# Kernel tuning notes

Hardware: AMD Instinct MI355X
Metric: run time of the kernel (lower is better)

The kernel has to match this reference:

```python
import jax, jax.numpy as jnp
import numpy as np

D = 1024   # n_embd
H = 16     # n_head
NL = 6     # n_layer
B = 16
L = 64
T = 3 * L  # interleaved (rtg, state, action) tokens
NB = 100   # rtg bucket number
DF = 4 * D


def _ln(x, g, b, eps=1e-5):
    mu = jnp.mean(x, -1, keepdims=True)
    var = jnp.mean((x - mu) ** 2, -1, keepdims=True)
    return (x - mu) * jax.lax.rsqrt(var + eps) * g + b


def _gelu(x):
    return jax.nn.gelu(x, approximate=False)  # matches torch F.gelu (erf)


def setup_inputs() -> dict:
    key = jax.random.key(0)
    ks = iter(jax.random.split(key, 64))
    def rn(shape, s=0.02):
        return jax.random.normal(next(ks), shape, jnp.float32) * s
    inp = dict(
        states=jax.random.normal(next(ks), (B, L, 91), jnp.float32),
        actions=jax.random.normal(next(ks), (B, L, 1, 27), jnp.float32),
        rtgs=jax.random.uniform(next(ks), (B, L), jnp.float32) * 100.0,
        attention_mask=jnp.ones((B, L), bool),
        y_len=L,
        # state encoder: Linear(91,D) GELU Linear(D,D) GELU
        se_w1=rn((91, D)), se_b1=jnp.zeros(D), se_w2=rn((D, D)), se_b2=jnp.zeros(D),
        # action encoder: Linear(27,D) GELU Linear(D,D)
        ae_w1=rn((27, D)), ae_b1=jnp.zeros(D), ae_w2=rn((D, D)), ae_b2=jnp.zeros(D),
        # Autodis
        ad_bucket_w=rn((1, D)), ad_bucket_b=jnp.zeros(D), ad_ret_w=rn((1, NB)), ad_res_w=rn((NB, NB)),
        pos_emb=rn((1, T, D)),
        # transformer blocks (stacked over layers)
        ln1_g=jnp.ones((NL, D)), ln1_b=jnp.zeros((NL, D)),
        Wq=rn((NL, D, D)), bq=jnp.zeros((NL, D)),
        Wk=rn((NL, D, D)), bk=jnp.zeros((NL, D)),
        Wv=rn((NL, D, D)), bv=jnp.zeros((NL, D)),
        Wp=rn((NL, D, D)), bp=jnp.zeros((NL, D)),
        ln2_g=jnp.ones((NL, D)), ln2_b=jnp.zeros((NL, D)),
        Wm1=rn((NL, D, DF)), bm1=jnp.zeros((NL, DF)),
        Wm2=rn((NL, DF, D)), bm2=jnp.zeros((NL, D)),
        lin_w=rn((D, 27)), lin_b=jnp.zeros(27),
    )
    return inp


def _forward(attention_mask, states, actions, rtgs, se_w1, se_b1, se_w2, se_b2,
             ae_w1, ae_b1, ae_w2, ae_b2, ad_bucket_w, ad_bucket_b, ad_ret_w, ad_res_w,
             pos_emb, ln1_g, ln1_b, Wq, bq, Wk, bk, Wv, bv, Wp, bp,
             ln2_g, ln2_b, Wm1, bm1, Wm2, bm2, lin_w, lin_b):
    Bsz, Ls = states.shape[0], states.shape[1]
    Ts = 3 * Ls
    hd = D // H
    # encoders
    state_emb = _gelu(_gelu(states @ se_w1 + se_b1) @ se_w2 + se_b2)          # [B,L,D]
    act = actions[:, :, 0, :]                                                  # squeeze(2) -> [B,L,27]
    action_emb = _gelu(act @ ae_w1 + ae_b1) @ ae_w2 + ae_b2                    # [B,L,D]
    # Autodis rtg embedding
    bucket_value = jnp.linspace(0.0, 100.0, NB).reshape(NB, 1)
    meta = bucket_value @ ad_bucket_w + ad_bucket_b                            # [NB,D]
    s = jax.nn.leaky_relu(rtgs[..., None] @ ad_ret_w)                          # [B,L,NB]
    s = s + s @ ad_res_w
    e = jnp.exp(s - jnp.max(s, -1, keepdims=True))
    p = e / (1e-8 + jnp.sum(e, -1, keepdims=True))
    rtg_emb = p @ meta                                                         # [B,L,D]
    # interleave rtg/state/action tokens -> [B,3L,D]
    tok = jnp.stack([rtg_emb, state_emb, action_emb], axis=2).reshape(Bsz, Ts, D)
    x = tok + pos_emb[:, :Ts]
    # combined padding + causal mask
    m = jnp.repeat(attention_mask, 3, axis=1)                                  # [B,3L]
    causal = jnp.tril(jnp.ones((Ts, Ts), bool))
    fmask = m[:, None, :, None] & m[:, None, None, :] & causal[None, None]     # [B,1,T,T]
    scale = 1.0 / np.sqrt(hd)
    for i in range(NL):
        h = _ln(x, ln1_g[i], ln1_b[i])
        q = (h @ Wq[i] + bq[i]).reshape(Bsz, Ts, H, hd).transpose(0, 2, 1, 3)
        k = (h @ Wk[i] + bk[i]).reshape(Bsz, Ts, H, hd).transpose(0, 2, 1, 3)
        v = (h @ Wv[i] + bv[i]).reshape(Bsz, Ts, H, hd).transpose(0, 2, 1, 3)
        att = jnp.einsum('bhid,bhjd->bhij', q, k) * scale
        att = jnp.where(fmask, att, -1e9)
        att = jax.nn.softmax(att, axis=-1)
        y = jnp.einsum('bhij,bhjd->bhid', att, v).transpose(0, 2, 1, 3).reshape(Bsz, Ts, D)
        x = x + (y @ Wp[i] + bp[i])
        h2 = _ln(x, ln2_g[i], ln2_b[i])
        x = x + _gelu(h2 @ Wm1[i] + bm1[i]) @ Wm2[i] + bm2[i]
    return x @ lin_w + lin_b                                                   # [B,3L,27]


def reference(states, actions, rtgs, attention_mask, y_len, se_w1, se_b1, se_w2, se_b2,
              ae_w1, ae_b1, ae_w2, ae_b2, ad_bucket_w, ad_bucket_b, ad_ret_w, ad_res_w,
              pos_emb, ln1_g, ln1_b, Wq, bq, Wk, bk, Wv, bv, Wp, bp,
              ln2_g, ln2_b, Wm1, bm1, Wm2, bm2, lin_w, lin_b):
    return _forward(attention_mask, states, actions, rtgs, se_w1, se_b1, se_w2, se_b2,
                    ae_w1, ae_b1, ae_w2, ae_b2, ad_bucket_w, ad_bucket_b, ad_ret_w, ad_res_w,
                    pos_emb, ln1_g, ln1_b, Wq, bq, Wk, bk, Wv, bv, Wp, bp,
                    ln2_g, ln2_b, Wm1, bm1, Wm2, bm2, lin_w, lin_b)
```

## Files before the change

### kernel.cpp

```cpp
#include <hip/hip_runtime.h>
#include <cmath>

typedef unsigned short u16;
typedef unsigned int   u32;
typedef short s16x8 __attribute__((ext_vector_type(8)));
typedef float f32x4 __attribute__((ext_vector_type(4)));

#define D_  1024
#define H_  16
#define NL_ 6
#define B_  16
#define L_  64
#define T_  192
#define NB_ 100
#define DF_ 4096
#define BT_ (B_*T_)
#define BL_ (B_*L_)

__device__ __forceinline__ float b2f(u16 u){ u32 x = ((u32)u)<<16; return __uint_as_float(x); }
__device__ __forceinline__ u16 f2b(float f){ u32 x = __float_as_uint(f); x += 0x7fffu + ((x>>16)&1u); return (u16)(x>>16); }
__device__ __forceinline__ float gelu_f(float v){ return 0.5f*v*(1.0f+erff(v*0.70710678118f)); }

typedef const unsigned int __attribute__((address_space(1)))* as1_u32p;
typedef unsigned int __attribute__((address_space(3)))* as3_u32p;
__device__ __forceinline__ void gload16(const void* g, void* l)
{
    __builtin_amdgcn_global_load_lds((as1_u32p)g, (as3_u32p)l, 16, 0, 0);
}

__device__ __forceinline__ void tconv_tile(const float* __restrict__ W,
                                           u16* __restrict__ Wt,
                                           int K, int N, int nb, int kb, int tid)
{
    __shared__ float tile[64][65];
    int tr = tid >> 4, tc = tid & 15;
#pragma unroll
    for (int rr = 0; rr < 4; ++rr) {
        int k = tr + rr*16;
        float4 v = *(const float4*)(W + (size_t)(kb + k)*N + nb + tc*4);
        tile[k][tc*4+0] = v.x; tile[k][tc*4+1] = v.y;
        tile[k][tc*4+2] = v.z; tile[k][tc*4+3] = v.w;
    }
    __syncthreads();
#pragma unroll
    for (int rr = 0; rr < 4; ++rr) {
        int n = tr + rr*16;
        ushort4 o;
        o.x = f2b(tile[tc*4+0][n]);
        o.y = f2b(tile[tc*4+1][n]);
        o.z = f2b(tile[tc*4+2][n]);
        o.w = f2b(tile[tc*4+3][n]);
        *(ushort4*)(Wt + (size_t)(nb + n)*K + kb + tc*4) = o;
    }
}

__global__ __launch_bounds__(256) void tconv_kernel(const float* __restrict__ W,
                                                    u16* __restrict__ Wt,
                                                    int K, int N)
{
    tconv_tile(W, Wt, K, N, blockIdx.x*64, blockIdx.y*64, threadIdx.x);
}

__global__ __launch_bounds__(256) void tconvL_kernel(const float* __restrict__ Wq,
                                                     const float* __restrict__ Wk,
                                                     const float* __restrict__ Wv,
                                                     const float* __restrict__ Wp,
                                                     const float* __restrict__ Wm1,
                                                     const float* __restrict__ Wm2,
                                                     u16* __restrict__ Wqkvt,
                                                     u16* __restrict__ Wpt,
                                                     u16* __restrict__ Wm1t,
                                                     u16* __restrict__ Wm2t,
                                                     int layer)
{
    size_t DD = (size_t)D_*D_, DDF = (size_t)D_*DF_;
    int t = blockIdx.x;
    if (t < 1024) {
        int sel = t >> 8, tt = t & 255;
        const float* Wz = ((sel == 0) ? Wq : (sel == 1) ? Wk : (sel == 2) ? Wv : Wp) + layer*DD;
        u16* Wtz = (sel == 3) ? (Wpt + layer*DD) : (Wqkvt + layer*3*DD + sel*DD);
        tconv_tile(Wz, Wtz, D_, D_, (tt & 15)*64, (tt >> 4)*64, threadIdx.x);
    } else if (t < 2048) {
        int t2 = t - 1024;
        tconv_tile(Wm1 + layer*DDF, Wm1t + layer*DDF, D_, DF_, (t2 & 63)*64, (t2 >> 6)*64, threadIdx.x);
    } else {
        int t2 = t - 2048;
        tconv_tile(Wm2 + layer*DDF, Wm2t + layer*DDF, DF_, D_, (t2 & 15)*64, (t2 >> 4)*64, threadIdx.x);
    }
}

__global__ __launch_bounds__(256) void pack_qkv_bias_kernel(const float* __restrict__ bq,
                                                            const float* __restrict__ bk,
                                                            const float* __restrict__ bv,
                                                            float* __restrict__ out)
{
    int i = blockIdx.x*256 + threadIdx.x;
    int layer = i / 3072;
    int r = i - layer*3072;
    int c = r >> 10, d = r & 1023;
    const float* src = (c == 0) ? bq : (c == 1) ? bk : bv;
    out[i] = src[layer*1024 + d];
}

__global__ __launch_bounds__(256) void tlin_kernel(const float* __restrict__ w,
                                                   float* __restrict__ wt)
{
    int k = blockIdx.x*256 + threadIdx.x;
#pragma unroll 1
    for (int c = 0; c < 27; ++c)
        wt[c*1024 + k] = w[k*27 + c];
}

__global__ __launch_bounds__(256) void embed1_kernel(const float* __restrict__ A,
                                                     const float* __restrict__ W,
                                                     const float* __restrict__ bias,
                                                     u16* __restrict__ out, int K)
{
    int idx = blockIdx.x*256 + threadIdx.x;
    int m = idx >> 10, n = idx & 1023;
    float acc = bias[n];
    for (int k = 0; k < K; ++k)
        acc += A[m*K + k] * W[k*1024 + n];
    out[idx] = f2b(gelu_f(acc));
}

__global__ __launch_bounds__(128) void rtg_kernel(const float* __restrict__ rtgs,
                                                  const float* __restrict__ ret_w,
                                                  const float* __restrict__ res_w,
                                                  const float* __restrict__ bucket_w,
                                                  const float* __restrict__ bucket_b,
                                                  float* __restrict__ eR)
{
    int r = blockIdx.x, tid = threadIdx.x;
    __shared__ float sarr[NB_];
    __shared__ float red[128];
    float rtg = rtgs[r];
    float s = 0.f;
    if (tid < NB_) {
        float v = rtg * ret_w[tid];
        s = (v > 0.f) ? v : 0.01f*v;
        sarr[tid] = s;
    }
    __syncthreads();
    float s2 = -1e30f;
    if (tid < NB_) {
        float acc = s;
        for (int m = 0; m < NB_; ++m) acc += sarr[m] * res_w[m*NB_ + tid];
        s2 = acc;
    }
    red[tid] = s2; __syncthreads();
    for (int off = 64; off > 0; off >>= 1) { if (tid < off) red[tid] = fmaxf(red[tid], red[tid+off]); __syncthreads(); }
    float mx = red[0]; __syncthreads();
    float e = (tid < NB_) ? expf(s2 - mx) : 0.f;
    red[tid] = e; __syncthreads();
    for (int off = 64; off > 0; off >>= 1) { if (tid < off) red[tid] += red[tid+off]; __syncthreads(); }
    float S = red[0]; __syncthreads();
    float bv = (100.f/99.f) * (float)tid;
    red[tid] = e * bv; __syncthreads();
    for (int off = 64; off > 0; off >>= 1) { if (tid < off) red[tid] += red[tid+off]; __syncthreads(); }
    float EB = red[0];
    float inv = 1.f/(1e-8f + S);
    float c = EB * inv, sg = S * inv;
    for (int d = tid; d < D_; d += 128)
        eR[(size_t)r*D_ + d] = c*bucket_w[d] + sg*bucket_b[d];
}

__global__ __launch_bounds__(256) void assemble_kernel(const float* __restrict__ eR,
                                                       const float* __restrict__ eS,
                                                       const float* __restrict__ eA,
                                                       const float* __restrict__ pos,
                                                       float* __restrict__ xf)
{
    int idx = blockIdx.x*256 + threadIdx.x;
    int row = idx >> 10, d = idx & 1023;
    int b = row / T_, t = row % T_;
    int l = t / 3, c = t % 3;
    const float* src = (c == 0) ? eR : (c == 1) ? eS : eA;
    xf[idx] = src[(size_t)(b*L_ + l)*D_ + d] + pos[(size_t)t*D_ + d];
}

template<int NP>
__global__ __launch_bounds__(256) void ln_kernel(const float* __restrict__ x,
                                                 const float* __restrict__ parts,
                                                 size_t pstride,
                                                 const float* __restrict__ g,
                                                 const float* __restrict__ bb,
                                                 float* __restrict__ xout,
                                                 u16* __restrict__ out)
{
    int row = blockIdx.x*4 + (threadIdx.x >> 6);
    int lane = threadIdx.x & 63;
    const float4* xr = (const float4*)(x + (size_t)row*D_);
    float4 v[4];
    float s = 0.f, q = 0.f;
#pragma unroll
    for (int i = 0; i < 4; ++i) {
        float4 a = xr[lane + i*64];
        if (NP == 4) {
#pragma unroll
            for (int z = 0; z < 4; ++z) {
                float4 p = ((const float4*)(parts + (size_t)z*pstride + (size_t)row*D_))[lane + i*64];
                a.x += p.x; a.y += p.y; a.z += p.z; a.w += p.w;
            }
        }
        v[i] = a;
        s += a.x+a.y+a.z+a.w;
        q += a.x*a.x+a.y*a.y+a.z*a.z+a.w*a.w;
    }
    if (NP == 4) {
#pragma unroll
        for (int i = 0; i < 4; ++i)
            ((float4*)(xout + (size_t)row*D_))[lane + i*64] = v[i];
    }
#pragma unroll
    for (int off = 1; off < 64; off <<= 1) {
        s += __shfl_xor(s, off, 64);
        q += __shfl_xor(q, off, 64);
    }
    float mean = s*(1.f/(float)D_);
    float var  = q*(1.f/(float)D_) - mean*mean;
    float rstd = rsqrtf(var + 1e-5f);
#pragma unroll
    for (int i = 0; i < 4; ++i) {
        int d0 = (lane + i*64)*4;
        ushort4 ov;
        ov.x = f2b((v[i].x-mean)*rstd*g[d0+0] + bb[d0+0]);
        ov.y = f2b((v[i].y-mean)*rstd*g[d0+1] + bb[d0+1]);
        ov.z = f2b((v[i].z-mean)*rstd*g[d0+2] + bb[d0+2]);
        ov.w = f2b((v[i].w-mean)*rstd*g[d0+3] + bb[d0+3]);
        ((ushort4*)(out + (size_t)row*D_))[lane + i*64] = ov;
    }
}

template<int GELU_ACT, int SPLITK, int ATOMIC>
__global__ __launch_bounds__(256) void gemm_bt(const u16* __restrict__ A,
                                               const u16* __restrict__ Bt,
                                               const float* __restrict__ bias,
                                               float* __restrict__ outF,
                                               u16* __restrict__ outB,
                                               int M, int N, int K, int kc,
                                               size_t partStride)
{
    __shared__ __align__(16) u16 As[3*128*32];
    __shared__ __align__(16) u16 Bs[3*128*32];
    int tid = threadIdx.x;

    int gx = gridDim.x;
    int nwg = gx * gridDim.y;
    int id = blockIdx.y * gx + blockIdx.x;
    int q8 = nwg >> 3;
    int nid = (id & 7) * q8 + (id >> 3);
    int n0 = (nid % gx) * 128;
    int m0 = (nid / gx) * 128;

    int wave = tid >> 6, lane = tid & 63;
    int wm = (wave >> 1) * 64, wn = (wave & 1) * 64;
    int lr = lane & 15, lq = lane >> 4;
    int slotRd = (lq ^ ((lr >> 1) & 3)) * 8;

    int srow = tid >> 2;
    int sslot = (tid & 3) ^ ((srow >> 1) & 3);

    int k0 = (SPLITK > 1) ? blockIdx.z * kc : 0;
    int nIt = ((SPLITK > 1) ? kc : K) >> 5;

    const u16* ap0 = A  + (size_t)(m0 + srow) * K + k0 + sslot * 8;
    const u16* ap1 = ap0 + (size_t)64 * K;
    const u16* bp0 = Bt + (size_t)(n0 + srow) * K + k0 + sslot * 8;
    const u16* bp1 = bp0 + (size_t)64 * K;

    u16 *sA0 = As, *sA1 = As + 4096, *sA2 = As + 8192;
    u16 *sB0 = Bs, *sB1 = Bs + 4096, *sB2 = Bs + 8192;
    int woff = wave * 512;

    f32x4 acc[4][4];
#pragma unroll
    for (int i = 0; i < 4; ++i)
#pragma unroll
        for (int j = 0; j < 4; ++j) acc[i][j] = (f32x4){0.f,0.f,0.f,0.f};

    gload16(ap0, sA0 + woff); gload16(ap1, sA0 + 2048 + woff);
    gload16(bp0, sB0 + woff); gload16(bp1, sB0 + 2048 + woff);
    ap0 += 32; ap1 += 32; bp0 += 32; bp1 += 32;
    gload16(ap0, sA1 + woff); gload16(ap1, sA1 + 2048 + woff);
    gload16(bp0, sB1 + woff); gload16(bp1, sB1 + 2048 + woff);
    ap0 += 32; ap1 += 32; bp0 += 32; bp1 += 32;

    for (int it = 0; it < nIt; ++it) {
        if (it + 1 < nIt) asm volatile("s_waitcnt vmcnt(4)" ::: "memory");
        else              asm volatile("s_waitcnt vmcnt(0)" ::: "memory");
        asm volatile("s_barrier" ::: "memory");
        if (it + 2 < nIt) {
            gload16(ap0, sA2 + woff); gload16(ap1, sA2 + 2048 + woff);
            gload16(bp0, sB2 + woff); gload16(bp1, sB2 + 2048 + woff);
            ap0 += 32; ap1 += 32; bp0 += 32; bp1 += 32;
        }
        s16x8 af[4], bf[4];
#pragma unroll
        for (int i = 0; i < 4; ++i)
            af[i] = *(const s16x8*)(sA0 + (wm + i*16 + lr)*32 + slotRd);
#pragma unroll
        for (int j = 0; j < 4; ++j)
            bf[j] = *(const s16x8*)(sB0 + (wn + j*16 + lr)*32 + slotRd);
#pragma unroll
        for (int i = 0; i < 4; ++i)
#pragma unroll
            for (int j = 0; j < 4; ++j)
                acc[i][j] = __builtin_amdgcn_mfma_f32_16x16x32_bf16(af[i], bf[j], acc[i][j], 0, 0, 0);
        u16* t0 = sA0; sA0 = sA1; sA1 = sA2; sA2 = t0;
        u16* t1 = sB0; sB0 = sB1; sB1 = sB2; sB2 = t1;
    }

    float* outZ = (SPLITK > 1 && !ATOMIC) ? outF + (size_t)blockIdx.z * partStride : outF;
#pragma unroll
    for (int i = 0; i < 4; ++i) {
        int mbase = m0 + wm + i*16 + lq*4;
#pragma unroll
        for (int j = 0; j < 4; ++j) {
            int n = n0 + wn + j*16 + lr;
            float bvl = (SPLITK > 1) ? ((blockIdx.z == 0) ? bias[n] : 0.f) : bias[n];
#pragma unroll
            for (int r = 0; r < 4; ++r) {
                int m = mbase + r;
                float v = acc[i][j][r] + bvl;
                size_t off = (size_t)m*N + n;
                if (SPLITK > 1) {
                    if (ATOMIC) atomicAdd(outF + off, v);
                    else        outZ[off] = v;
                } else {
                    if (GELU_ACT) v = gelu_f(v);
                    if (outF) outF[off] = v;
                    if (outB) outB[off] = f2b(v);
                }
            }
        }
    }
}

__global__ __launch_bounds__(256) void attn_mfma_kernel(const u16* __restrict__ qkv,
                                                        u16* __restrict__ yb)
{
    __shared__ __align__(16) u16 Vt[64*200];
    __shared__ __align__(16) u16 Pch[4][16*40];

    int tid = threadIdx.x;
    int b = blockIdx.x >> 4, h = blockIdx.x & 15;
    int c = blockIdx.y;
    int nrows = (c + 1) * 64;
    int bT = b * T_;
    int colBase = h * 64;
    int w = tid >> 6, lane = tid & 63;
    int lr = lane & 15, lq = lane >> 4;
    const int S3 = 3 * D_;

    for (int it = 0; it < (nrows >> 5); ++it) {
        int cc = it*256 + tid;
        int row = cc >> 3, ch = cc & 7;
        union { int4 v; u16 s[8]; } rv;
        rv.v = *(const int4*)(qkv + (size_t)(bT+row)*S3 + 2*D_ + colBase + ch*8);
#pragma unroll
        for (int i2 = 0; i2 < 8; ++i2)
            Vt[(ch*8 + i2)*200 + row] = rv.s[i2];
    }

    u16* Ch = Pch[w];
    int qt = c*4 + w;
    int tqb = qt * 16;

    const u16* qrow = qkv + (size_t)(bT + tqb + lr)*S3 + colBase + lq*8;
    s16x8 af0 = *(const s16x8*)(qrow);
    s16x8 af1 = *(const s16x8*)(qrow + 32);

    f32x4 sacc[12];
#pragma unroll
    for (int jt = 0; jt < 12; ++jt) {
        if (jt <= qt) {
            const u16* kr = qkv + (size_t)(bT + jt*16 + lr)*S3 + D_ + colBase + lq*8;
            s16x8 bk0 = *(const s16x8*)(kr);
            s16x8 bk1 = *(const s16x8*)(kr + 32);
            f32x4 a = (f32x4){0.f,0.f,0.f,0.f};
            a = __builtin_amdgcn_mfma_f32_16x16x32_bf16(af0, bk0, a, 0, 0, 0);
            a = __builtin_amdgcn_mfma_f32_16x16x32_bf16(af1, bk1, a, 0, 0, 0);
            sacc[jt] = a;
        }
    }

    float mrow[4] = {-1e30f,-1e30f,-1e30f,-1e30f};
#pragma unroll
    for (int jt = 0; jt < 12; ++jt) if (jt <= qt) {
#pragma unroll
        for (int r = 0; r < 4; ++r) {
            bool valid = (jt < qt) || (lr <= lq*4 + r);
            float s = valid ? sacc[jt][r]*0.125f : -1e30f;
            sacc[jt][r] = s;
            mrow[r] = fmaxf(mrow[r], s);
        }
    }
#pragma unroll
    for (int r = 0; r < 4; ++r) {
#pragma unroll
        for (int off = 1; off < 16; off <<= 1)
            mrow[r] = fmaxf(mrow[r], __shfl_xor(mrow[r], off, 64));
    }

    float lrow[4] = {0.f,0.f,0.f,0.f};
#pragma unroll
    for (int jt = 0; jt < 12; ++jt) if (jt <= qt) {
#pragma unroll
        for (int r = 0; r < 4; ++r) {
            float e = __expf(sacc[jt][r] - mrow[r]);
            sacc[jt][r] = e;
            lrow[r] += e;
        }
    }
#pragma unroll
    for (int r = 0; r < 4; ++r) {
#pragma unroll
        for (int off = 1; off < 16; off <<= 1)
            lrow[r] += __shfl_xor(lrow[r], off, 64);
        lrow[r] = 1.f / lrow[r];
    }

    __syncthreads();

    int nkt = (qt + 2) >> 1;
    f32x4 oacc[4];
#pragma unroll
    for (int nt = 0; nt < 4; ++nt) oacc[nt] = (f32x4){0.f,0.f,0.f,0.f};

#pragma unroll
    for (int kt = 0; kt < 6; ++kt) if (kt < nkt) {
        int jt0 = 2*kt, jt1 = 2*kt + 1;
#pragma unroll
        for (int r = 0; r < 4; ++r) {
            u16 e0 = f2b(sacc[jt0][r]);
            u16 e1 = (jt1 <= qt) ? f2b(sacc[jt1][r]) : (u16)0;
            Ch[(lq*4 + r)*40 + lr]      = e0;
            Ch[(lq*4 + r)*40 + 16 + lr] = e1;
        }
        s16x8 ap = *(const s16x8*)(Ch + lr*40 + lq*8);
#pragma unroll
        for (int nt = 0; nt < 4; ++nt) {
            s16x8 bv = *(const s16x8*)(Vt + (nt*16 + lr)*200 + kt*32 + lq*8);
            oacc[nt] = __builtin_amdgcn_mfma_f32_16x16x32_bf16(ap, bv, oacc[nt], 0, 0, 0);
        }
    }

#pragma unroll
    for (int nt = 0; nt < 4; ++nt)
#pragma unroll
        for (int r = 0; r < 4; ++r)
            yb[(size_t)(bT + tqb + lq*4 + r)*D_ + colBase + nt*16 + lr] =
                f2b(oacc[nt][r] * lrow[r]);
}

template<int NP>
__global__ __launch_bounds__(256) void final_kernel(const float* __restrict__ xf,
                                                    const float* __restrict__ parts,
                                                    size_t pstride,
                                                    const float* __restrict__ lin_wT,
                                                    const float* __restrict__ lin_b,
                                                    float* __restrict__ out)
{
    int row = blockIdx.x*4 + (threadIdx.x >> 6);
    int lane = threadIdx.x & 63;
    const float4* xr = (const float4*)(xf + (size_t)row*D_);
    float4 x[4];
#pragma unroll
    for (int i = 0; i < 4; ++i) {
        float4 v = xr[lane + i*64];
        if (NP == 4) {
#pragma unroll
            for (int z = 0; z < 4; ++z) {
                float4 p = ((const float4*)(parts + (size_t)z*pstride + (size_t)row*D_))[lane + i*64];
                v.x += p.x; v.y += p.y; v.z += p.z; v.w += p.w;
            }
        }
        x[i] = v;
    }
#pragma unroll 1
    for (int c = 0; c < 27; ++c) {
        const float4* wr = (const float4*)(lin_wT + (size_t)c*D_);
        float a = 0.f;
#pragma unroll
        for (int i = 0; i < 4; ++i) {
            float4 wv = wr[lane + i*64];
            a += x[i].x*wv.x + x[i].y*wv.y + x[i].z*wv.z + x[i].w*wv.w;
        }
#pragma unroll
        for (int off = 1; off < 64; off <<= 1)
            a += __shfl_xor(a, off, 64);
        if (lane == 0) out[(size_t)row*27 + c] = a + lin_b[c];
    }
}

extern "C" void kernel_launch(void* const* d_in, const int* in_sizes, int n_in,
                              void* d_out, int out_size, void* d_ws, size_t ws_size,
                              hipStream_t stream)
{
    const float* states   = (const float*)d_in[0];
    const float* actions  = (const float*)d_in[1];
    const float* rtgs     = (const float*)d_in[2];
    const float* se_w1 = (const float*)d_in[5];
    const float* se_b1 = (const float*)d_in[6];
    const float* se_w2 = (const float*)d_in[7];
    const float* se_b2 = (const float*)d_in[8];
    const float* ae_w1 = (const float*)d_in[9];
    const float* ae_b1 = (const float*)d_in[10];
    const float* ae_w2 = (const float*)d_in[11];
    const float* ae_b2 = (const float*)d_in[12];
    const float* ad_bucket_w = (const float*)d_in[13];
    const float* ad_bucket_b = (const float*)d_in[14];
    const float* ad_ret_w = (const float*)d_in[15];
    const float* ad_res_w = (const float*)d_in[16];
    const float* pos_emb  = (const float*)d_in[17];
    const float* ln1_g = (const float*)d_in[18];
    const float* ln1_b = (const float*)d_in[19];
    const float* Wq = (const float*)d_in[20];
    const float* bq = (const float*)d_in[21];
    const float* Wk = (const float*)d_in[22];
    const float* bk = (const float*)d_in[23];
    const float* Wv = (const float*)d_in[24];
    const float* bv = (const float*)d_in[25];
    const float* Wp = (const float*)d_in[26];
    const float* bp = (const float*)d_in[27];
    const float* ln2_g = (const float*)d_in[28];
    const float* ln2_b = (const float*)d_in[29];
    const float* Wm1 = (const float*)d_in[30];
    const float* bm1 = (const float*)d_in[31];
    const float* Wm2 = (const float*)d_in[32];
    const float* bm2 = (const float*)d_in[33];
    const float* lin_w = (const float*)d_in[34];
    const float* lin_b = (const float*)d_in[35];

    char* w = (char*)d_ws;
    auto take = [&](size_t bytes) { char* p = w; w += (bytes + 255) & ~(size_t)255; return p; };

    float* xf   = (float*)take((size_t)BT_*D_*4);
    u16* hb     = (u16*)take((size_t)BT_*D_*2);
    u16* qkvb   = (u16*)take((size_t)BT_*3*D_*2);
    char* scr   =        take((size_t)BT_*DF_*2);
    u16*  midb  = (u16*)scr;
    u16*  tSb   = (u16*)scr;
    u16*  tAb   = (u16*)(scr + (size_t)BL_*D_*2);
    float* eS   = (float*)(scr + (size_t)2*BL_*D_*2);
    float* eA   = (float*)(scr + (size_t)2*BL_*D_*2 + (size_t)BL_*D_*4);
    float* eR   = (float*)(scr + (size_t)2*BL_*D_*2 + (size_t)2*BL_*D_*4);
    float* pp   = (float*)take((size_t)4*BT_*D_*4);
    float* mq   = (float*)take((size_t)4*BT_*D_*4);

    u16* Wqkvt = (u16*)take((size_t)NL_*3*D_*D_*2);
    u16* Wpt   = (u16*)take((size_t)NL_*D_*D_*2);
    u16* Wm1t  = (u16*)take((size_t)NL_*D_*DF_*2);
    u16* Wm2t  = (u16*)take((size_t)NL_*DF_*D_*2);
    u16* sw2t  = (u16*)take((size_t)D_*D_*2);
    u16* aw2t  = (u16*)take((size_t)D_*D_*2);
    float* bqkv= (float*)take((size_t)NL_*3*D_*4);
    float* lwT = (float*)take((size_t)27*D_*4);

    size_t ask = (size_t)(w - (char*)d_ws);
    bool bigWS = (ws_size >= ask);

    const size_t PSTRIDE = (size_t)BT_*D_;
    size_t DD = (size_t)D_*D_, DDF = (size_t)D_*DF_;

    pack_qkv_bias_kernel<<<72, 256, 0, stream>>>(bq, bk, bv, bqkv);
    tlin_kernel<<<4, 256, 0, stream>>>(lin_w, lwT);
    tconv_kernel<<<dim3(16,16), 256, 0, stream>>>(se_w2, sw2t, D_, D_);
    tconv_kernel<<<dim3(16,16), 256, 0, stream>>>(ae_w2, aw2t, D_, D_);
    tconvL_kernel<<<3072, 256, 0, stream>>>(Wq, Wk, Wv, Wp, Wm1, Wm2,
                                            Wqkvt, Wpt, Wm1t, Wm2t, 0);

    embed1_kernel<<<4096, 256, 0, stream>>>(states,  se_w1, se_b1, tSb, 91);
    embed1_kernel<<<4096, 256, 0, stream>>>(actions, ae_w1, ae_b1, tAb, 27);
    gemm_bt<1,1,0><<<dim3(8,8), 256, 0, stream>>>(tSb, sw2t, se_b2, eS, nullptr, BL_, D_, D_, D_, 0);
    gemm_bt<0,1,0><<<dim3(8,8), 256, 0, stream>>>(tAb, aw2t, ae_b2, eA, nullptr, BL_, D_, D_, D_, 0);
    rtg_kernel<<<BL_, 128, 0, stream>>>(rtgs, ad_ret_w, ad_res_w, ad_bucket_w, ad_bucket_b, eR);
    assemble_kernel<<<(BT_*D_)/256, 256, 0, stream>>>(eR, eS, eA, pos_emb, xf);

    for (int i = 0; i < NL_; ++i) {
        if (i > 0 && bigWS)
            ln_kernel<4><<<BT_/4, 256, 0, stream>>>(xf, mq, PSTRIDE, ln1_g + i*D_, ln1_b + i*D_, xf, hb);
        else
            ln_kernel<0><<<BT_/4, 256, 0, stream>>>(xf, nullptr, 0, ln1_g + i*D_, ln1_b + i*D_, nullptr, hb);
        gemm_bt<0,1,0><<<dim3(24,24), 256, 0, stream>>>(hb, Wqkvt + (size_t)i*3*DD, bqkv + i*3*D_,
                                                        nullptr, qkvb, BT_, 3*D_, D_, D_, 0);
        attn_mfma_kernel<<<dim3(B_*H_,3), 256, 0, stream>>>(qkvb, hb);
        if (i + 1 < NL_)
            tconvL_kernel<<<3072, 256, 0, stream>>>(Wq, Wk, Wv, Wp, Wm1, Wm2,
                                                    Wqkvt, Wpt, Wm1t, Wm2t, i+1);
        if (bigWS)
            gemm_bt<0,4,0><<<dim3(8,24,4), 256, 0, stream>>>(hb, Wpt + (size_t)i*DD, bp + i*D_,
                                                             pp, nullptr, BT_, D_, D_, 256, PSTRIDE);
        else
            gemm_bt<0,2,1><<<dim3(8,24,2), 256, 0, stream>>>(hb, Wpt + (size_t)i*DD, bp + i*D_,
                                                             xf, nullptr, BT_, D_, D_, 512, 0);
        if (bigWS)
            ln_kernel<4><<<BT_/4, 256, 0, stream>>>(xf, pp, PSTRIDE, ln2_g + i*D_, ln2_b + i*D_, xf, hb);
        else
            ln_kernel<0><<<BT_/4, 256, 0, stream>>>(xf, nullptr, 0, ln2_g + i*D_, ln2_b + i*D_, nullptr, hb);
        gemm_bt<1,1,0><<<dim3(32,24), 256, 0, stream>>>(hb, Wm1t + (size_t)i*DDF, bm1 + i*DF_,
                                                        nullptr, midb, BT_, DF_, D_, D_, 0);
        if (bigWS)
            gemm_bt<0,4,0><<<dim3(8,24,4), 256, 0, stream>>>(midb, Wm2t + (size_t)i*DDF, bm2 + i*D_,
                                                             mq, nullptr, BT_, D_, DF_, 1024, PSTRIDE);
        else
            gemm_bt<0,2,1><<<dim3(8,24,2), 256, 0, stream>>>(midb, Wm2t + (size_t)i*DDF, bm2 + i*D_,
                                                             xf, nullptr, BT_, D_, DF_, 2048, 0);
    }

    if (bigWS)
        final_kernel<4><<<BT_/4, 256, 0, stream>>>(xf, mq, PSTRIDE, lwT, lin_b, (float*)d_out);
    else
        final_kernel<0><<<BT_/4, 256, 0, stream>>>(xf, nullptr, 0, lwT, lin_b, (float*)d_out);
}
```

Before: 1.557 ms.

## Store split-K partials in bf16 and stage attention K tile in LDS

```diff
diff --git a/kernel.cpp b/kernel.cpp
--- a/kernel.cpp
+++ b/kernel.cpp
@@ -181,7 +181,7 @@
 
 template<int NP>
 __global__ __launch_bounds__(256) void ln_kernel(const float* __restrict__ x,
-                                                 const float* __restrict__ parts,
+                                                 const u16* __restrict__ parts,
                                                  size_t pstride,
                                                  const float* __restrict__ g,
                                                  const float* __restrict__ bb,
@@ -199,8 +199,8 @@
         if (NP == 4) {
 #pragma unroll
             for (int z = 0; z < 4; ++z) {
-                float4 p = ((const float4*)(parts + (size_t)z*pstride + (size_t)row*D_))[lane + i*64];
-                a.x += p.x; a.y += p.y; a.z += p.z; a.w += p.w;
+                ushort4 p = ((const ushort4*)(parts + (size_t)z*pstride + (size_t)row*D_))[lane + i*64];
+                a.x += b2f(p.x); a.y += b2f(p.y); a.z += b2f(p.z); a.w += b2f(p.w);
             }
         }
         v[i] = a;
@@ -311,7 +311,7 @@
         u16* t1 = sB0; sB0 = sB1; sB1 = sB2; sB2 = t1;
     }
 
-    float* outZ = (SPLITK > 1 && !ATOMIC) ? outF + (size_t)blockIdx.z * partStride : outF;
+    u16* outZ = (SPLITK > 1 && !ATOMIC) ? outB + (size_t)blockIdx.z * partStride : outB;
 #pragma unroll
     for (int i = 0; i < 4; ++i) {
         int mbase = m0 + wm + i*16 + lq*4;
@@ -326,7 +326,7 @@
                 size_t off = (size_t)m*N + n;
                 if (SPLITK > 1) {
                     if (ATOMIC) atomicAdd(outF + off, v);
-                    else        outZ[off] = v;
+                    else        outZ[off] = f2b(v);
                 } else {
                     if (GELU_ACT) v = gelu_f(v);
                     if (outF) outF[off] = v;
@@ -340,6 +340,7 @@
 __global__ __launch_bounds__(256) void attn_mfma_kernel(const u16* __restrict__ qkv,
                                                         u16* __restrict__ yb)
 {
+    __shared__ __align__(16) u16 Ks[192*72];
     __shared__ __align__(16) u16 Vt[64*200];
     __shared__ __align__(16) u16 Pch[4][16*40];
 
@@ -356,12 +357,15 @@
     for (int it = 0; it < (nrows >> 5); ++it) {
         int cc = it*256 + tid;
         int row = cc >> 3, ch = cc & 7;
+        *(int4*)(Ks + row*72 + ch*8) =
+            *(const int4*)(qkv + (size_t)(bT+row)*S3 + D_ + colBase + ch*8);
         union { int4 v; u16 s[8]; } rv;
         rv.v = *(const int4*)(qkv + (size_t)(bT+row)*S3 + 2*D_ + colBase + ch*8);
 #pragma unroll
         for (int i2 = 0; i2 < 8; ++i2)
             Vt[(ch*8 + i2)*200 + row] = rv.s[i2];
     }
+    __syncthreads();
 
     u16* Ch = Pch[w];
     int qt = c*4 + w;
@@ -375,9 +379,8 @@
 #pragma unroll
     for (int jt = 0; jt < 12; ++jt) {
         if (jt <= qt) {
-            const u16* kr = qkv + (size_t)(bT + jt*16 + lr)*S3 + D_ + colBase + lq*8;
-            s16x8 bk0 = *(const s16x8*)(kr);
-            s16x8 bk1 = *(const s16x8*)(kr + 32);
+            s16x8 bk0 = *(const s16x8*)(Ks + (jt*16 + lr)*72 + lq*8);
+            s16x8 bk1 = *(const s16x8*)(Ks + (jt*16 + lr)*72 + 32 + lq*8);
             f32x4 a = (f32x4){0.f,0.f,0.f,0.f};
             a = __builtin_amdgcn_mfma_f32_16x16x32_bf16(af0, bk0, a, 0, 0, 0);
             a = __builtin_amdgcn_mfma_f32_16x16x32_bf16(af1, bk1, a, 0, 0, 0);
@@ -421,8 +424,6 @@
         lrow[r] = 1.f / lrow[r];
     }
 
-    __syncthreads();
-
     int nkt = (qt + 2) >> 1;
     f32x4 oacc[4];
 #pragma unroll
@@ -456,7 +457,7 @@
 
 template<int NP>
 __global__ __launch_bounds__(256) void final_kernel(const float* __restrict__ xf,
-                                                    const float* __restrict__ parts,
+                                                    const u16* __restrict__ parts,
                                                     size_t pstride,
                                                     const float* __restrict__ lin_wT,
                                                     const float* __restrict__ lin_b,
@@ -472,8 +473,8 @@
         if (NP == 4) {
 #pragma unroll
             for (int z = 0; z < 4; ++z) {
-                float4 p = ((const float4*)(parts + (size_t)z*pstride + (size_t)row*D_))[lane + i*64];
-                v.x += p.x; v.y += p.y; v.z += p.z; v.w += p.w;
+                ushort4 p = ((const ushort4*)(parts + (size_t)z*pstride + (size_t)row*D_))[lane + i*64];
+                v.x += b2f(p.x); v.y += b2f(p.y); v.z += b2f(p.z); v.w += b2f(p.w);
             }
         }
         x[i] = v;
@@ -546,8 +547,8 @@
     float* eS   = (float*)(scr + (size_t)2*BL_*D_*2);
     float* eA   = (float*)(scr + (size_t)2*BL_*D_*2 + (size_t)BL_*D_*4);
     float* eR   = (float*)(scr + (size_t)2*BL_*D_*2 + (size_t)2*BL_*D_*4);
-    float* pp   = (float*)take((size_t)4*BT_*D_*4);
-    float* mq   = (float*)take((size_t)4*BT_*D_*4);
+    u16* pp     = (u16*)take((size_t)4*BT_*D_*2);
+    u16* mq     = (u16*)take((size_t)4*BT_*D_*2);
 
     u16* Wqkvt = (u16*)take((size_t)NL_*3*D_*D_*2);
     u16* Wpt   = (u16*)take((size_t)NL_*D_*D_*2);
@@ -591,7 +592,7 @@
                                                     Wqkvt, Wpt, Wm1t, Wm2t, i+1);
         if (bigWS)
             gemm_bt<0,4,0><<<dim3(8,24,4), 256, 0, stream>>>(hb, Wpt + (size_t)i*DD, bp + i*D_,
-                                                             pp, nullptr, BT_, D_, D_, 256, PSTRIDE);
+                                                             nullptr, pp, BT_, D_, D_, 256, PSTRIDE);
         else
             gemm_bt<0,2,1><<<dim3(8,24,2), 256, 0, stream>>>(hb, Wpt + (size_t)i*DD, bp + i*D_,
                                                              xf, nullptr, BT_, D_, D_, 512, 0);
@@ -603,7 +604,7 @@
                                                         nullptr, midb, BT_, DF_, D_, D_, 0);
         if (bigWS)
             gemm_bt<0,4,0><<<dim3(8,24,4), 256, 0, stream>>>(midb, Wm2t + (size_t)i*DDF, bm2 + i*D_,
-                                                             mq, nullptr, BT_, D_, DF_, 1024, PSTRIDE);
+                                                             nullptr, mq, BT_, D_, DF_, 1024, PSTRIDE);
         else
             gemm_bt<0,2,1><<<dim3(8,24,2), 256, 0, stream>>>(midb, Wm2t + (size_t)i*DDF, bm2 + i*D_,
                                                              xf, nullptr, BT_, D_, DF_, 2048, 0);
```

Measured after the change: 1.489 ms. 1.05x faster.
